# Kernel tuning notes

Measured on AMD Instinct MI355X. Metric: run time of the kernel, lower is better.

The kernel has to match this reference:

```python
import jax, jax.numpy as jnp
import numpy as np

NUM_HEADS = 16
D_MODEL = 1024
HEAD_DIM = D_MODEL // NUM_HEADS
B, S = 2, 2048


def setup_inputs() -> dict:
    key = jax.random.key(0)
    ks = jax.random.split(key, 11)
    scale = 1.0 / np.sqrt(D_MODEL)
    inp = {
        'query': jax.random.normal(ks[0], (B, S, D_MODEL), jnp.float32),
        'key': jax.random.normal(ks[1], (B, S, D_MODEL), jnp.float32),
        'value': jax.random.normal(ks[2], (B, S, D_MODEL), jnp.float32),
        'Wq': jax.random.normal(ks[3], (D_MODEL, D_MODEL), jnp.float32) * scale,
        'bq': jnp.zeros((D_MODEL,), jnp.float32),
        'Wk': jax.random.normal(ks[4], (D_MODEL, D_MODEL), jnp.float32) * scale,
        'bk': jnp.zeros((D_MODEL,), jnp.float32),
        'Wv': jax.random.normal(ks[5], (D_MODEL, D_MODEL), jnp.float32) * scale,
        'bv': jnp.zeros((D_MODEL,), jnp.float32),
        'Wo': jax.random.normal(ks[6], (D_MODEL, D_MODEL), jnp.float32) * scale,
        'bo': jnp.zeros((D_MODEL,), jnp.float32),
    }
    return inp


def reference(query, key, value, Wq, bq, Wk, bk, Wv, bv, Wo, bo):
    b, s, _ = query.shape
    # Linear projections (torch Linear: x @ W.T + b; here W stored as [in,out])
    Q = query @ Wq + bq
    K = key @ Wk + bk
    V = value @ Wv + bv
    # [B, H, S, Dh]
    Q = Q.reshape(b, s, NUM_HEADS, HEAD_DIM).transpose(0, 2, 1, 3)
    K = K.reshape(b, -1, NUM_HEADS, HEAD_DIM).transpose(0, 2, 1, 3)
    V = V.reshape(b, -1, NUM_HEADS, HEAD_DIM).transpose(0, 2, 1, 3)
    scores = jnp.einsum('bhqd,bhkd->bhqk', Q, K) / jnp.sqrt(jnp.float32(HEAD_DIM)).astype(Q.dtype)
    attn = jax.nn.softmax(scores, axis=-1)
    ctx = jnp.einsum('bhqk,bhkd->bhqd', attn, V)
    ctx = ctx.transpose(0, 2, 1, 3).reshape(b, s, D_MODEL)
    return ctx @ Wo + bo
```

## Files before the change

kernel.cpp:

```cpp
#include <hip/hip_runtime.h>
#include <hip/hip_bf16.h>
#include <math.h>

#define NUM_HEADS 16
#define D_MODEL 1024
#define HEAD_DIM 64
#define BATCH 2
#define SEQ 2048
#define M_TOTAL (BATCH*SEQ)

typedef __bf16 bf16;
typedef __bf16 bf16x2 __attribute__((ext_vector_type(2)));
typedef __bf16 bf16x4 __attribute__((ext_vector_type(4)));
typedef __bf16 bf16x8 __attribute__((ext_vector_type(8)));
typedef float  floatx4  __attribute__((ext_vector_type(4)));
typedef float  floatx16 __attribute__((ext_vector_type(16)));
typedef unsigned int uintx4 __attribute__((ext_vector_type(4)));

#define CLSCALE 0.180336884f

#if __has_builtin(__builtin_amdgcn_exp2f)
#define EXP2(x) __builtin_amdgcn_exp2f(x)
#else
#define EXP2(x) exp2f(x)
#endif

__device__ __forceinline__ void async_copy16(const bf16* g, bf16* l) {
    __builtin_amdgcn_global_load_lds(
        (const __attribute__((address_space(1))) void*)g,
        (__attribute__((address_space(3))) void*)l, 16, 0, 0);
}

__device__ __forceinline__ unsigned pk2(float lo, float hi) {
    bf16x2 t; t[0] = (bf16)lo; t[1] = (bf16)hi;
    return __builtin_bit_cast(unsigned, t);
}

__global__ __launch_bounds__(256)
void convert_kernel(const float* __restrict__ Wq, const float* __restrict__ Wk,
                    const float* __restrict__ Wv, const float* __restrict__ Wo,
                    const float* __restrict__ q, const float* __restrict__ k,
                    const float* __restrict__ v,
                    bf16* __restrict__ Wt, bf16* __restrict__ Xb)
{
    const int blk = blockIdx.x;
    const int tid = threadIdx.x;
    if (blk < 256) {
        const int wi  = blk >> 6;
        const int sub = blk & 63;
        const int xb  = sub & 3;
        const int yb  = sub >> 2;
        const float* W = (wi == 0) ? Wq : (wi == 1) ? Wk : (wi == 2) ? Wv : Wo;
        bf16* dstM = Wt + (size_t)wi * D_MODEL * D_MODEL;
        const int n  = xb * 256 + tid;
        const int k0 = yb * 64;
        bf16* dst = dstM + (size_t)n * D_MODEL + k0;
        #pragma unroll
        for (int jc = 0; jc < 8; ++jc) {
            bf16x8 w;
            #pragma unroll
            for (int j = 0; j < 8; ++j)
                w[j] = (bf16)W[(size_t)(k0 + jc * 8 + j) * D_MODEL + n];
            *(bf16x8*)(dst + jc * 8) = w;
        }
    } else {
        const int rem   = blk - 256;
        const int plane = rem >> 11;
        const int xb    = rem & 2047;
        const float* X = (plane == 0) ? q : (plane == 1) ? k : v;
        bf16* dst = Xb + (size_t)plane * M_TOTAL * D_MODEL;
        size_t i = ((size_t)xb * 256 + tid) * 8;
        const float4 u = *(const float4*)(X + i);
        const float4 w = *(const float4*)(X + i + 4);
        bf16x8 o;
        o[0] = (bf16)u.x; o[1] = (bf16)u.y; o[2] = (bf16)u.z; o[3] = (bf16)u.w;
        o[4] = (bf16)w.x; o[5] = (bf16)w.y; o[6] = (bf16)w.z; o[7] = (bf16)w.w;
        *(bf16x8*)(dst + i) = o;
    }
}

__global__ __launch_bounds__(256)
void proj_kernel(const bf16* __restrict__ Xb, const bf16* __restrict__ Wt,
                 const float* __restrict__ bq, const float* __restrict__ bk,
                 const float* __restrict__ bv,
                 bf16* __restrict__ Qo, bf16* __restrict__ Ko, bf16* __restrict__ Vto)
{
    const int lin  = blockIdx.x;
    const int xcd  = lin & 7;
    const int idx  = lin >> 3;
    const int nt   = idx & 7;
    const int t2   = idx >> 3;
    const int mloc = t2 & 3;
    const int which= t2 >> 2;
    const int tileM = (xcd * 4 + mloc) * 128;
    const int tileN = nt * 128;

    const bf16* X     = Xb + (size_t)which * M_TOTAL * D_MODEL;
    const bf16* Wm    = Wt + (size_t)which * D_MODEL * D_MODEL;
    const float* bias = (which == 0) ? bq : (which == 1) ? bk : bv;

    const int tid  = threadIdx.x;
    const int lane = tid & 63;
    const int wave = tid >> 6;
    const int quad = lane >> 4;
    const int l16  = lane & 15;

    __shared__ bf16 sA[128 * 32];
    __shared__ bf16 sB[128 * 32];

    floatx4 acc[4][4];
    const floatx4 z4 = {0.0f, 0.0f, 0.0f, 0.0f};
    #pragma unroll
    for (int i = 0; i < 4; i++)
        #pragma unroll
        for (int j = 0; j < 4; j++) acc[i][j] = z4;

    const int wm = (wave >> 1) * 64;
    const int wn = (wave & 1) * 64;

    const int c0   = wave * 64 + lane;
    const int row0 = c0 >> 2, col0 = (c0 & 3) * 8;
    const int c1   = c0 + 256;
    const int row1 = c1 >> 2, col1 = (c1 & 3) * 8;
    bf16* ldsA0 = sA + (size_t)(wave * 64) * 8;
    bf16* ldsA1 = sA + (size_t)(256 + wave * 64) * 8;
    bf16* ldsB0 = sB + (size_t)(wave * 64) * 8;
    bf16* ldsB1 = sB + (size_t)(256 + wave * 64) * 8;

    for (int k0 = 0; k0 < D_MODEL; k0 += 32) {
        __syncthreads();
        async_copy16(X  + (size_t)(tileM + row0) * D_MODEL + k0 + col0, ldsA0);
        async_copy16(X  + (size_t)(tileM + row1) * D_MODEL + k0 + col1, ldsA1);
        async_copy16(Wm + (size_t)(tileN + row0) * D_MODEL + k0 + col0, ldsB0);
        async_copy16(Wm + (size_t)(tileN + row1) * D_MODEL + k0 + col1, ldsB1);
        __syncthreads();

        bf16x8 af[4], bfr[4];
        #pragma unroll
        for (int i = 0; i < 4; i++) af[i]  = *(const bf16x8*)&sA[(wm + i * 16 + l16) * 32 + quad * 8];
        #pragma unroll
        for (int j = 0; j < 4; j++) bfr[j] = *(const bf16x8*)&sB[(wn + j * 16 + l16) * 32 + quad * 8];
        if (which != 2) {
            #pragma unroll
            for (int i = 0; i < 4; i++)
                #pragma unroll
                for (int j = 0; j < 4; j++)
                    acc[i][j] = __builtin_amdgcn_mfma_f32_16x16x32_bf16(af[i], bfr[j], acc[i][j], 0, 0, 0);
        } else {
            #pragma unroll
            for (int i = 0; i < 4; i++)
                #pragma unroll
                for (int j = 0; j < 4; j++)
                    acc[i][j] = __builtin_amdgcn_mfma_f32_16x16x32_bf16(bfr[i], af[j], acc[i][j], 0, 0, 0);
        }
    }

    if (which != 2) {
        bf16* out = (which == 0) ? Qo : Ko;
        const float oscale = (which == 0) ? CLSCALE : 1.0f;
        #pragma unroll
        for (int i = 0; i < 4; i++) {
            int mbase = tileM + wm + i * 16 + quad * 4;
            #pragma unroll
            for (int j = 0; j < 4; j++) {
                int n = tileN + wn + j * 16 + l16;
                float bb = bias[n];
                int h = n >> 6, d = n & 63;
                #pragma unroll
                for (int r = 0; r < 4; r++) {
                    int mm = mbase + r;
                    int b = mm >> 11, s = mm & 2047;
                    out[(((size_t)(b * NUM_HEADS + h)) * SEQ + s) * HEAD_DIM + d] =
                        (bf16)((acc[i][j][r] + bb) * oscale);
                }
            }
        }
    } else {
        #pragma unroll
        for (int i = 0; i < 4; i++) {
            #pragma unroll
            for (int r = 0; r < 4; r++) {
                int n = tileN + wn + i * 16 + quad * 4 + r;
                float bb = bias[n];
                int h = n >> 6, d = n & 63;
                #pragma unroll
                for (int j = 0; j < 4; j++) {
                    int m = tileM + wm + j * 16 + l16;
                    int b = m >> 11, s = m & 2047;
                    Vto[(((size_t)(b * NUM_HEADS + h)) * HEAD_DIM + d) * SEQ + s] =
                        (bf16)(acc[i][j][r] + bb);
                }
            }
        }
    }
}

__global__ __launch_bounds__(512)
void attn_kernel(const bf16* __restrict__ Q, const bf16* __restrict__ K,
                 const bf16* __restrict__ Vt, bf16* __restrict__ Ctx)
{
    const int lin    = blockIdx.x;
    const int xcd    = lin & 7;
    const int rest   = lin >> 3;
    const int superg = rest >> 4;
    const int qi     = rest & 15;
    const int bh     = superg * 8 + xcd;
    const int b      = bh >> 4, h = bh & 15;
    const int q0     = qi * 128;

    const int tid  = threadIdx.x;
    const int lane = tid & 63;
    const int wave = tid >> 6;
    const int half = lane >> 5;
    const int m31  = lane & 31;
    const int xs   = m31 & 7;

    const int qsub  = wave & 3;
    const int kjsub = wave >> 2;

    __shared__ bf16 sK[2][64 * 64];
    __shared__ bf16 sV[2][64 * 64];
    __shared__ float sL[128];

    const bf16* Qb  = Q  + ((size_t)bh * SEQ + q0) * HEAD_DIM;
    const bf16* Kb  = K  + (size_t)bh * SEQ * HEAD_DIM;
    const bf16* Vtb = Vt + (size_t)bh * HEAD_DIM * SEQ;

    bf16x8 bQ[4];
    #pragma unroll
    for (int s = 0; s < 4; s++)
        bQ[s] = *(const bf16x8*)(Qb + (size_t)(qsub * 32 + m31) * HEAD_DIM + s * 16 + half * 8);

    {
        const int c    = tid;
        const int row  = c >> 3;
        const int scol = ((c & 7) ^ (row & 7)) * 8;
        async_copy16(Kb  + (size_t)row * HEAD_DIM + scol, &sK[0][c * 8]);
        async_copy16(Vtb + (size_t)row * SEQ + scol,      &sV[0][c * 8]);
    }

    floatx16 o0, o1;
    #pragma unroll
    for (int r = 0; r < 16; r++) { o0[r] = 0.0f; o1[r] = 0.0f; }
    float lp = 0.0f;

    for (int kt = 0; kt < SEQ / 64; ++kt) {
        const int p = kt & 1;
        __syncthreads();

        bf16x8 aK[4];
        #pragma unroll
        for (int s = 0; s < 4; s++)
            aK[s] = *(const bf16x8*)&sK[p][(kjsub * 32 + m31) * 64 + (((2 * s + half) ^ xs) * 8)];

        if (kt + 1 < SEQ / 64) {
            const int c    = tid;
            const int row  = c >> 3;
            const int scol = ((c & 7) ^ (row & 7)) * 8;
            async_copy16(Kb  + (size_t)((kt + 1) * 64 + row) * HEAD_DIM + scol,
                         &sK[p ^ 1][c * 8]);
            async_copy16(Vtb + (size_t)row * SEQ + (kt + 1) * 64 + scol,
                         &sV[p ^ 1][c * 8]);
        }

        floatx16 sc;
        #pragma unroll
        for (int r = 0; r < 16; r++) sc[r] = 0.0f;
        __builtin_amdgcn_s_setprio(1);
        #pragma unroll
        for (int s = 0; s < 4; s++)
            sc = __builtin_amdgcn_mfma_f32_32x32x16_bf16(aK[s], bQ[s], sc, 0, 0, 0);
        __builtin_amdgcn_s_setprio(0);

        #pragma unroll
        for (int r = 0; r < 16; r++) sc[r] = EXP2(sc[r]);
        float t0 = (sc[0] + sc[1]) + (sc[2] + sc[3]);
        float t1 = (sc[4] + sc[5]) + (sc[6] + sc[7]);
        float t2 = (sc[8] + sc[9]) + (sc[10] + sc[11]);
        float t3 = (sc[12] + sc[13]) + (sc[14] + sc[15]);
        lp += (t0 + t1) + (t2 + t3);

        bf16x8 bP[2];
        #pragma unroll
        for (int s = 0; s < 2; s++) {
            const int bs = 8 * s;
            unsigned x = pk2(sc[bs + 0], sc[bs + 1]);
            unsigned z = pk2(sc[bs + 2], sc[bs + 3]);
            unsigned y = pk2(sc[bs + 4], sc[bs + 5]);
            unsigned w = pk2(sc[bs + 6], sc[bs + 7]);
            auto r0 = __builtin_amdgcn_permlane32_swap(x, y, false, false);
            auto r1 = __builtin_amdgcn_permlane32_swap(z, w, false, false);
            uintx4 bp;
            bp[0] = r0[0]; bp[1] = r1[0]; bp[2] = r0[1]; bp[3] = r1[1];
            bP[s] = __builtin_bit_cast(bf16x8, bp);
        }

        __builtin_amdgcn_s_setprio(1);
        #pragma unroll
        for (int s = 0; s < 2; s++) {
            int ch = ((4 * kjsub + 2 * s + half) ^ xs) * 8;
            bf16x8 a0 = *(const bf16x8*)&sV[p][(size_t)m31 * 64 + ch];
            bf16x8 a1 = *(const bf16x8*)&sV[p][(size_t)(32 + m31) * 64 + ch];
            o0 = __builtin_amdgcn_mfma_f32_32x32x16_bf16(a0, bP[s], o0, 0, 0, 0);
            o1 = __builtin_amdgcn_mfma_f32_32x32x16_bf16(a1, bP[s], o1, 0, 0, 0);
        }
        __builtin_amdgcn_s_setprio(0);
    }

    lp += __shfl_xor(lp, 32, 64);

    __syncthreads();
    float* fO = (qsub == 0) ? (float*)&sK[0][0] :
                (qsub == 1) ? (float*)&sK[1][0] :
                (qsub == 2) ? (float*)&sV[0][0] : (float*)&sV[1][0];
    if (kjsub == 1) {
        #pragma unroll
        for (int r = 0; r < 16; r++) {
            fO[r * 64 + lane]        = o0[r];
            fO[1024 + r * 64 + lane] = o1[r];
        }
        if (half == 0) sL[qsub * 32 + m31] = lp;
    }
    __syncthreads();
    if (kjsub == 0) {
        #pragma unroll
        for (int r = 0; r < 16; r++) {
            o0[r] += fO[r * 64 + lane];
            o1[r] += fO[1024 + r * 64 + lane];
        }
        float denom = lp + sL[qsub * 32 + m31];
        float inv = 1.0f / denom;

        int q = q0 + qsub * 32 + m31;
        size_t base = ((size_t)b * SEQ + q) * D_MODEL + h * HEAD_DIM;
        #pragma unroll
        for (int rg = 0; rg < 4; rg++) {
            int d0 = rg * 8 + half * 4;
            bf16x4 w0, w1;
            #pragma unroll
            for (int i = 0; i < 4; i++) {
                w0[i] = (bf16)(o0[rg * 4 + i] * inv);
                w1[i] = (bf16)(o1[rg * 4 + i] * inv);
            }
            *(bf16x4*)&Ctx[base + d0]      = w0;
            *(bf16x4*)&Ctx[base + 32 + d0] = w1;
        }
    }
}

__global__ __launch_bounds__(256)
void out_proj_kernel(const bf16* __restrict__ A, const bf16* __restrict__ Wto,
                     const float* __restrict__ bias, float* __restrict__ Out)
{
    const int lin  = blockIdx.x;
    const int xcd  = lin & 7;
    const int idx  = lin >> 3;
    const int nt   = idx & 15;
    const int mloc = idx >> 4;
    const int tileM = (xcd * 4 + mloc) * 128;
    const int tileN = nt * 64;

    const int tid  = threadIdx.x;
    const int lane = tid & 63;
    const int wave = tid >> 6;
    const int quad = lane >> 4;
    const int l16  = lane & 15;

    __shared__ bf16 sA[128 * 32];
    __shared__ bf16 sB[64 * 32];

    floatx4 acc[4][2];
    const floatx4 z4 = {0.0f, 0.0f, 0.0f, 0.0f};
    #pragma unroll
    for (int i = 0; i < 4; i++)
        #pragma unroll
        for (int j = 0; j < 2; j++) acc[i][j] = z4;

    const int wm = (wave >> 1) * 64;
    const int wn = (wave & 1) * 32;

    const int c0   = wave * 64 + lane;
    const int row0 = c0 >> 2, col0 = (c0 & 3) * 8;
    const int c1   = c0 + 256;
    const int row1 = c1 >> 2, col1 = (c1 & 3) * 8;
    bf16* ldsA0 = sA + (size_t)(wave * 64) * 8;
    bf16* ldsA1 = sA + (size_t)(256 + wave * 64) * 8;
    bf16* ldsB0 = sB + (size_t)(wave * 64) * 8;

    for (int k0 = 0; k0 < D_MODEL; k0 += 32) {
        __syncthreads();
        async_copy16(A   + (size_t)(tileM + row0) * D_MODEL + k0 + col0, ldsA0);
        async_copy16(A   + (size_t)(tileM + row1) * D_MODEL + k0 + col1, ldsA1);
        async_copy16(Wto + (size_t)(tileN + row0) * D_MODEL + k0 + col0, ldsB0);
        __syncthreads();

        bf16x8 af[4], bfr[2];
        #pragma unroll
        for (int i = 0; i < 4; i++) af[i]  = *(const bf16x8*)&sA[(wm + i * 16 + l16) * 32 + quad * 8];
        #pragma unroll
        for (int j = 0; j < 2; j++) bfr[j] = *(const bf16x8*)&sB[(wn + j * 16 + l16) * 32 + quad * 8];

        #pragma unroll
        for (int i = 0; i < 4; i++)
            #pragma unroll
            for (int j = 0; j < 2; j++)
                acc[i][j] = __builtin_amdgcn_mfma_f32_16x16x32_bf16(af[i], bfr[j], acc[i][j], 0, 0, 0);
    }

    #pragma unroll
    for (int i = 0; i < 4; i++) {
        int mbase = tileM + wm + i * 16 + quad * 4;
        #pragma unroll
        for (int j = 0; j < 2; j++) {
            int n = tileN + wn + j * 16 + l16;
            float bb = bias[n];
            #pragma unroll
            for (int r = 0; r < 4; r++)
                Out[(size_t)(mbase + r) * D_MODEL + n] = acc[i][j][r] + bb;
        }
    }
}

extern "C" void kernel_launch(void* const* d_in, const int* in_sizes, int n_in,
                              void* d_out, int out_size, void* d_ws, size_t ws_size,
                              hipStream_t stream)
{
    const float* q  = (const float*)d_in[0];
    const float* k  = (const float*)d_in[1];
    const float* v  = (const float*)d_in[2];
    const float* Wq = (const float*)d_in[3];
    const float* bq = (const float*)d_in[4];
    const float* Wk = (const float*)d_in[5];
    const float* bk = (const float*)d_in[6];
    const float* Wv = (const float*)d_in[7];
    const float* bv = (const float*)d_in[8];
    const float* Wo = (const float*)d_in[9];
    const float* bo = (const float*)d_in[10];
    float* out = (float*)d_out;

    const size_t PLANE = (size_t)M_TOTAL * D_MODEL;
    bf16* Qb = (bf16*)d_ws;
    bf16* Kb = Qb + PLANE;
    bf16* Vt = Kb + PLANE;
    bf16* Cb = Vt + PLANE;
    bf16* Wt = Cb + PLANE;
    bf16* Xb = Wt + 4 * (size_t)D_MODEL * D_MODEL;

    convert_kernel<<<dim3(6400), 256, 0, stream>>>(Wq, Wk, Wv, Wo, q, k, v, Wt, Xb);
    proj_kernel<<<dim3(768), 256, 0, stream>>>(Xb, Wt, bq, bk, bv, Qb, Kb, Vt);
    attn_kernel<<<dim3(512), 512, 0, stream>>>(Qb, Kb, Vt, Cb);
    out_proj_kernel<<<dim3(512), 256, 0, stream>>>(Cb, Wt + 3 * (size_t)D_MODEL * D_MODEL, bo, out);
}
```

Baseline: 228.2 us.

## Fuse fp32-to-bf16 activation conversion into the QKV projection GEMM

```diff
diff --git a/kernel.cpp b/kernel.cpp
--- a/kernel.cpp
+++ b/kernel.cpp
@@ -25,7 +25,7 @@
 #define EXP2(x) exp2f(x)
 #endif
 
-__device__ __forceinline__ void async_copy16(const bf16* g, bf16* l) {
+__device__ __forceinline__ void async_copy16(const void* g, void* l) {
     __builtin_amdgcn_global_load_lds(
         (const __attribute__((address_space(1))) void*)g,
         (__attribute__((address_space(3))) void*)l, 16, 0, 0);
@@ -39,48 +39,32 @@
 __global__ __launch_bounds__(256)
 void convert_kernel(const float* __restrict__ Wq, const float* __restrict__ Wk,
                     const float* __restrict__ Wv, const float* __restrict__ Wo,
-                    const float* __restrict__ q, const float* __restrict__ k,
-                    const float* __restrict__ v,
-                    bf16* __restrict__ Wt, bf16* __restrict__ Xb)
+                    bf16* __restrict__ Wt)
 {
     const int blk = blockIdx.x;
     const int tid = threadIdx.x;
-    if (blk < 256) {
-        const int wi  = blk >> 6;
-        const int sub = blk & 63;
-        const int xb  = sub & 3;
-        const int yb  = sub >> 2;
-        const float* W = (wi == 0) ? Wq : (wi == 1) ? Wk : (wi == 2) ? Wv : Wo;
-        bf16* dstM = Wt + (size_t)wi * D_MODEL * D_MODEL;
-        const int n  = xb * 256 + tid;
-        const int k0 = yb * 64;
-        bf16* dst = dstM + (size_t)n * D_MODEL + k0;
-        #pragma unroll
-        for (int jc = 0; jc < 8; ++jc) {
-            bf16x8 w;
-            #pragma unroll
-            for (int j = 0; j < 8; ++j)
-                w[j] = (bf16)W[(size_t)(k0 + jc * 8 + j) * D_MODEL + n];
-            *(bf16x8*)(dst + jc * 8) = w;
-        }
-    } else {
-        const int rem   = blk - 256;
-        const int plane = rem >> 11;
-        const int xb    = rem & 2047;
-        const float* X = (plane == 0) ? q : (plane == 1) ? k : v;
-        bf16* dst = Xb + (size_t)plane * M_TOTAL * D_MODEL;
-        size_t i = ((size_t)xb * 256 + tid) * 8;
-        const float4 u = *(const float4*)(X + i);
-        const float4 w = *(const float4*)(X + i + 4);
-        bf16x8 o;
-        o[0] = (bf16)u.x; o[1] = (bf16)u.y; o[2] = (bf16)u.z; o[3] = (bf16)u.w;
-        o[4] = (bf16)w.x; o[5] = (bf16)w.y; o[6] = (bf16)w.z; o[7] = (bf16)w.w;
-        *(bf16x8*)(dst + i) = o;
+    const int wi  = blk >> 6;
+    const int sub = blk & 63;
+    const int xb  = sub & 3;
+    const int yb  = sub >> 2;
+    const float* W = (wi == 0) ? Wq : (wi == 1) ? Wk : (wi == 2) ? Wv : Wo;
+    bf16* dstM = Wt + (size_t)wi * D_MODEL * D_MODEL;
+    const int n  = xb * 256 + tid;
+    const int k0 = yb * 64;
+    bf16* dst = dstM + (size_t)n * D_MODEL + k0;
+    #pragma unroll
+    for (int jc = 0; jc < 8; ++jc) {
+        bf16x8 w;
+        #pragma unroll
+        for (int j = 0; j < 8; ++j)
+            w[j] = (bf16)W[(size_t)(k0 + jc * 8 + j) * D_MODEL + n];
+        *(bf16x8*)(dst + jc * 8) = w;
     }
 }
 
 __global__ __launch_bounds__(256)
-void proj_kernel(const bf16* __restrict__ Xb, const bf16* __restrict__ Wt,
+void proj_kernel(const float* __restrict__ Xq, const float* __restrict__ Xk,
+                 const float* __restrict__ Xv, const bf16* __restrict__ Wt,
                  const float* __restrict__ bq, const float* __restrict__ bk,
                  const float* __restrict__ bv,
                  bf16* __restrict__ Qo, bf16* __restrict__ Ko, bf16* __restrict__ Vto)
@@ -95,7 +79,7 @@
     const int tileM = (xcd * 4 + mloc) * 128;
     const int tileN = nt * 128;
 
-    const bf16* X     = Xb + (size_t)which * M_TOTAL * D_MODEL;
+    const float* X32  = (which == 0) ? Xq : (which == 1) ? Xk : Xv;
     const bf16* Wm    = Wt + (size_t)which * D_MODEL * D_MODEL;
     const float* bias = (which == 0) ? bq : (which == 1) ? bk : bv;
 
@@ -105,8 +89,8 @@
     const int quad = lane >> 4;
     const int l16  = lane & 15;
 
-    __shared__ bf16 sA[128 * 32];
-    __shared__ bf16 sB[128 * 32];
+    __shared__ float sA4[128 * 32];
+    __shared__ bf16  sB[128 * 32];
 
     floatx4 acc[4][4];
     const floatx4 z4 = {0.0f, 0.0f, 0.0f, 0.0f};
@@ -119,27 +103,44 @@
     const int wn = (wave & 1) * 64;
 
     const int c0   = wave * 64 + lane;
-    const int row0 = c0 >> 2, col0 = (c0 & 3) * 8;
+    const int rowB0 = c0 >> 2, colB0 = (c0 & 3) * 8;
     const int c1   = c0 + 256;
-    const int row1 = c1 >> 2, col1 = (c1 & 3) * 8;
-    bf16* ldsA0 = sA + (size_t)(wave * 64) * 8;
-    bf16* ldsA1 = sA + (size_t)(256 + wave * 64) * 8;
+    const int rowB1 = c1 >> 2, colB1 = (c1 & 3) * 8;
     bf16* ldsB0 = sB + (size_t)(wave * 64) * 8;
     bf16* ldsB1 = sB + (size_t)(256 + wave * 64) * 8;
 
     for (int k0 = 0; k0 < D_MODEL; k0 += 32) {
         __syncthreads();
-        async_copy16(X  + (size_t)(tileM + row0) * D_MODEL + k0 + col0, ldsA0);
-        async_copy16(X  + (size_t)(tileM + row1) * D_MODEL + k0 + col1, ldsA1);
-        async_copy16(Wm + (size_t)(tileN + row0) * D_MODEL + k0 + col0, ldsB0);
-        async_copy16(Wm + (size_t)(tileN + row1) * D_MODEL + k0 + col1, ldsB1);
+
+        #pragma unroll
+        for (int it = 0; it < 4; ++it) {
+            const int c   = tid + 256 * it;
+            const int row = c >> 3;
+            const int sc  = ((c & 7) ^ (row & 7)) * 4;
+            async_copy16(X32 + (size_t)(tileM + row) * D_MODEL + k0 + sc,
+                         sA4 + (size_t)c * 4);
+        }
+        async_copy16(Wm + (size_t)(tileN + rowB0) * D_MODEL + k0 + colB0, ldsB0);
+        async_copy16(Wm + (size_t)(tileN + rowB1) * D_MODEL + k0 + colB1, ldsB1);
+
         __syncthreads();
 
         bf16x8 af[4], bfr[4];
         #pragma unroll
-        for (int i = 0; i < 4; i++) af[i]  = *(const bf16x8*)&sA[(wm + i * 16 + l16) * 32 + quad * 8];
+        for (int i = 0; i < 4; i++) {
+            const int R  = wm + i * 16 + l16;
+            const int j0 = (2 * quad)     ^ (R & 7);
+            const int j1 = (2 * quad + 1) ^ (R & 7);
+            float4 u = *(const float4*)&sA4[(size_t)(R * 8 + j0) * 4];
+            float4 v = *(const float4*)&sA4[(size_t)(R * 8 + j1) * 4];
+            uintx4 t;
+            t[0] = pk2(u.x, u.y); t[1] = pk2(u.z, u.w);
+            t[2] = pk2(v.x, v.y); t[3] = pk2(v.z, v.w);
+            af[i] = __builtin_bit_cast(bf16x8, t);
+        }
         #pragma unroll
         for (int j = 0; j < 4; j++) bfr[j] = *(const bf16x8*)&sB[(wn + j * 16 + l16) * 32 + quad * 8];
+
         if (which != 2) {
             #pragma unroll
             for (int i = 0; i < 4; i++)
@@ -444,10 +445,9 @@
     bf16* Vt = Kb + PLANE;
     bf16* Cb = Vt + PLANE;
     bf16* Wt = Cb + PLANE;
-    bf16* Xb = Wt + 4 * (size_t)D_MODEL * D_MODEL;
-
-    convert_kernel<<<dim3(6400), 256, 0, stream>>>(Wq, Wk, Wv, Wo, q, k, v, Wt, Xb);
-    proj_kernel<<<dim3(768), 256, 0, stream>>>(Xb, Wt, bq, bk, bv, Qb, Kb, Vt);
+
+    convert_kernel<<<dim3(256), 256, 0, stream>>>(Wq, Wk, Wv, Wo, Wt);
+    proj_kernel<<<dim3(768), 256, 0, stream>>>(q, k, v, Wt, bq, bk, bv, Qb, Kb, Vt);
     attn_kernel<<<dim3(512), 512, 0, stream>>>(Qb, Kb, Vt, Cb);
     out_proj_kernel<<<dim3(512), 256, 0, stream>>>(Cb, Wt + 3 * (size_t)D_MODEL * D_MODEL, bo, out);
 }
```

Measured after the change: 251.9 us. 10.4% more time.
